# Kernel tuning notes

Hardware: AMD Instinct MI355X
Metric: run time of the kernel (lower is better)

The kernel has to match this reference:

```python
import jax, jax.numpy as jnp
from jax import lax
import numpy as np

C = 256
K = 3
PAD = 1


def _bilinear_sample(x, py, px):
    """Zero-padded bilinear sampling.
    x: [B,C,Hin,Win]; py,px: [B,Kt,H,W] float sample coords -> [B,C,Kt,H,W]."""
    B, Cc, Hin, Win = x.shape
    y0 = jnp.floor(py)
    x0 = jnp.floor(px)
    y1 = y0 + 1.0
    x1 = x0 + 1.0
    wy1 = py - y0
    wy0 = 1.0 - wy1
    wx1 = px - x0
    wx0 = 1.0 - wx1
    xf = x.reshape(B, Cc, Hin * Win)

    def corner(yi, xi, wy, wx):
        valid = (yi >= 0) & (yi < Hin) & (xi >= 0) & (xi < Win)
        yc = jnp.clip(yi, 0, Hin - 1).astype(jnp.int32)
        xc = jnp.clip(xi, 0, Win - 1).astype(jnp.int32)
        idx = yc * Win + xc  # [B,Kt,H,W]
        g = jax.vmap(lambda xb, ib: xb[:, ib])(xf, idx)  # [B,C,Kt,H,W]
        w = (wy * wx) * valid.astype(x.dtype)
        return g * w[:, None]

    return (corner(y0, x0, wy0, wx0) + corner(y0, x1, wy0, wx1)
            + corner(y1, x0, wy1, wx0) + corner(y1, x1, wy1, wx1))


def _arm_forward(x, w_off, b_off, w, b):
    B, Cc, H, W = x.shape
    # offset-predicting conv (standard 3x3, pad 1)
    off = lax.conv_general_dilated(
        x, w_off, window_strides=(1, 1), padding=[(PAD, PAD), (PAD, PAD)],
        dimension_numbers=('NCHW', 'OIHW', 'NCHW')) + b_off[None, :, None, None]
    off = off.reshape(B, K * K, 2, H, W)  # [:, k, 0]=dy, [:, k, 1]=dx (mmcv layout)
    ky, kx = jnp.meshgrid(jnp.arange(K), jnp.arange(K), indexing='ij')
    ky = ky.reshape(-1).astype(x.dtype)  # [9]
    kx = kx.reshape(-1).astype(x.dtype)
    base_y = jnp.arange(H, dtype=x.dtype)[None, None, :, None]
    base_x = jnp.arange(W, dtype=x.dtype)[None, None, None, :]
    py = base_y - PAD + ky[None, :, None, None] + off[:, :, 0]  # [B,9,H,W]
    px = base_x - PAD + kx[None, :, None, None] + off[:, :, 1]
    sampled = _bilinear_sample(x, py, px)  # [B,C,9,H,W]
    out = jnp.einsum('bckhw,ock->bohw', sampled, w.reshape(Cc, Cc, K * K))
    out = out + b[None, :, None, None]
    return jax.nn.sigmoid(out)


def setup_inputs() -> dict:
    key = jax.random.key(0)
    k1, k2, k3, k4 = jax.random.split(key, 4)
    B, H, W = 8, 64, 64
    x = jax.random.normal(k1, (B, C, H, W), dtype=jnp.float32)
    # offset conv params (mmcv zero-inits these; use small random to exercise sampling)
    w_off = jax.random.normal(k2, (2 * K * K, C, K, K), dtype=jnp.float32) * 0.01
    b_off = jnp.zeros((2 * K * K,), dtype=jnp.float32)
    # deformable conv weight/bias (kaiming-ish scale)
    scale = 1.0 / np.sqrt(C * K * K)
    w = jax.random.normal(k3, (C, C, K, K), dtype=jnp.float32) * scale
    b = jax.random.normal(k4, (C,), dtype=jnp.float32) * scale
    return {"Fstagei": x, "w_off": w_off, "b_off": b_off, "w": w, "b": b}


def reference(Fstagei, w_off, b_off, w, b):
    return _arm_forward(Fstagei, w_off, b_off, w, b)
```

## Files before the change

kernel.cpp:

```cpp
#include <hip/hip_runtime.h>

typedef unsigned short u16;
typedef unsigned int u32;
typedef __attribute__((ext_vector_type(8))) short short8;
typedef __attribute__((ext_vector_type(4))) float f32x4;

#define BB 8
#define CCH 256
#define HH 64
#define WW 64
#define HP 66
#define NPOS 4096
#define KTOT 2304

#define XT_BYTES   17842176ull
#define W2R_OFF    17842176ull
#define WOFF2_OFF  19021824ull
#define P_OFF      19169280ull
#define OFF2_OFF   40402944ull
#define WS_MIN     42762240ull

__device__ __forceinline__ float bf2f(u16 u) {
    union { u32 u; float f; } v; v.u = ((u32)u) << 16; return v.f;
}
__device__ __forceinline__ u16 f2bf(float f) {
    union { float f; u32 u; } v; v.f = f;
    u32 r = v.u + 0x7FFFu + ((v.u >> 16) & 1u);
    return (u16)(r >> 16);
}
__device__ __forceinline__ u32 pk2(float a, float b) {
    return (u32)f2bf(a) | ((u32)f2bf(b) << 16);
}
__device__ __forceinline__ u32 cvtpk(float lo, float hi) {
    u32 r;
    asm("v_cvt_pk_bf16_f32 %0, %1, %2" : "=v"(r) : "v"(lo), "v"(hi));
    return r;
}
__device__ __forceinline__ void bf2x2(u32 p, float& a, float& b) {
    union { u32 u; float f; } va, vb;
    va.u = p << 16; vb.u = p & 0xffff0000u;
    a = va.f; b = vb.f;
}
__device__ __forceinline__ void ldg_lds16(const u16* g, u16* l) {
    __builtin_amdgcn_global_load_lds((const __attribute__((address_space(1))) u32*)g,
                                     (__attribute__((address_space(3))) u32*)l, 16, 0, 0);
}

__global__ __launch_bounds__(256) void k_pre(const float* __restrict__ w, const float* __restrict__ w_off,
                                             const float* __restrict__ x,
                                             u16* __restrict__ W2r, u16* __restrict__ Woff2,
                                             u16* __restrict__ xT) {
    __shared__ __align__(16) float SH[4608];
    int bx = blockIdx.x;
    int t = threadIdx.x;
    if (bx < 256) {
        int o = bx;
        const float* src = w + (size_t)o * 2304;
#pragma unroll
        for (int j = 0; j < 9; ++j) SH[j * 256 + t] = src[j * 256 + t];
        __syncthreads();
        u16* dst = W2r + (size_t)o * 2304;
#pragma unroll
        for (int k = 0; k < 9; ++k) dst[k * 256 + t] = f2bf(SH[t * 9 + k]);
    } else if (bx == 256) {
        for (int o2 = 0; o2 < 32; ++o2) {
            if (o2 < 18) {
                const float* src = w_off + (size_t)o2 * 2304;
#pragma unroll
                for (int j = 0; j < 9; ++j) SH[j * 256 + t] = src[j * 256 + t];
                __syncthreads();
#pragma unroll
                for (int k = 0; k < 9; ++k) Woff2[(size_t)o2 * 2304 + k * 256 + t] = f2bf(SH[t * 9 + k]);
                __syncthreads();
            } else {
#pragma unroll
                for (int k = 0; k < 9; ++k) Woff2[(size_t)o2 * 2304 + k * 256 + t] = 0;
            }
        }
    } else if (bx < 777) {
        int idx = (bx - 257) * 4 + (t >> 6);
        int b = idx / 260, m = idx - b * 260;
        int y, xx;
        if (m < 66)       { y = 0;  xx = m; }
        else if (m < 132) { y = 65; xx = m - 66; }
        else if (m < 196) { y = m - 132 + 1; xx = 0; }
        else              { y = m - 196 + 1; xx = 65; }
        u16* p = xT + ((size_t)(b * HP + y) * HP + xx) * CCH + (t & 63) * 4;
        uint2 zz; zz.x = 0; zz.y = 0;
        *(uint2*)p = zz;
    } else {
        int idx = bx - 777;
        int b = idx & 7;
        int r = idx >> 3;
        int y = r & 63, c0 = (r >> 6) * 64;
        {
            int i = t >> 2, seg = t & 3;
            const float* src = x + (((size_t)(b * CCH + c0 + i) * HH + y) * WW) + seg * 16;
            float4 v0 = *(const float4*)(src);
            float4 v1 = *(const float4*)(src + 4);
            float4 v2 = *(const float4*)(src + 8);
            float4 v3 = *(const float4*)(src + 12);
            *(float4*)&SH[i * 72 + seg * 16]      = v0;
            *(float4*)&SH[i * 72 + seg * 16 + 4]  = v1;
            *(float4*)&SH[i * 72 + seg * 16 + 8]  = v2;
            *(float4*)&SH[i * 72 + seg * 16 + 12] = v3;
        }
        __syncthreads();
        {
            int xc = t >> 2, cs = t & 3;
            u16* dst = xT + (((size_t)(b * HP + y + 1) * HP) + (xc + 1)) * CCH + c0 + cs * 16;
            u32 p[8];
#pragma unroll
            for (int j = 0; j < 8; ++j)
                p[j] = pk2(SH[(cs * 16 + 2 * j) * 72 + xc], SH[(cs * 16 + 2 * j + 1) * 72 + xc]);
            uint4 d0, d1;
            d0.x = p[0]; d0.y = p[1]; d0.z = p[2]; d0.w = p[3];
            d1.x = p[4]; d1.y = p[5]; d1.z = p[6]; d1.w = p[7];
            *(uint4*)dst = d0;
            *(uint4*)(dst + 8) = d1;
        }
    }
}

__global__ __launch_bounds__(256) void k_offconv(const u16* __restrict__ xT,
                                                 const u16* __restrict__ Woff2,
                                                 float* __restrict__ P) {
    __shared__ __align__(16) u16 AS[2][2048];
    __shared__ __align__(16) u16 BS[2][8192];
    int b = blockIdx.x, k9 = blockIdx.y;
    int pos0 = blockIdx.z * 128;
    int ky = k9 / 3, kx = k9 % 3;
    int t = threadIdx.x, lane = t & 63, wv = t >> 6;

    int srow = lane >> 3;
    int sw8 = ((lane & 7) ^ srow) << 3;
    const u16* pA = Woff2 + (size_t)k9 * 256;
    const u16* pXb = xT + (size_t)b * HP * HP * CCH;

    f32x4 acc[2][2];
    f32x4 z = {0.f, 0.f, 0.f, 0.f};
    acc[0][0] = z; acc[0][1] = z; acc[1][0] = z; acc[1][1] = z;

    auto stage = [&](int cs, int d) {
        int koff = cs * 64;
        {
            int row = wv * 8 + srow;
            ldg_lds16(pA + (size_t)row * KTOT + koff + sw8, &AS[d][wv * 512]);
        }
#pragma unroll
        for (int i = 0; i < 4; ++i) {
            int inst = wv * 4 + i;
            int rowg = pos0 + inst * 8 + srow;
            int py_ = rowg >> 6, px_ = rowg & 63;
            const u16* g = pXb + (((size_t)(py_ + ky) * HP) + px_ + kx) * CCH + koff + sw8;
            ldg_lds16(g, &BS[d][inst * 512]);
        }
    };

    stage(0, 0);
    __syncthreads();

    int buf = 0;
    int m = lane & 15, q = lane >> 4, key = lane & 7;
    for (int cs = 0; cs < 4; ++cs) {
        if (cs < 3) stage(cs + 1, buf ^ 1);
#pragma unroll
        for (int j = 0; j < 2; ++j) {
            int slot8 = (((j * 4 + q) ^ key) << 3);
            short8 a0 = *(const short8*)&AS[buf][m * 64 + slot8];
            short8 a1 = *(const short8*)&AS[buf][(16 + m) * 64 + slot8];
            short8 b0 = *(const short8*)&BS[buf][(wv * 32 + m) * 64 + slot8];
            short8 b1 = *(const short8*)&BS[buf][(wv * 32 + 16 + m) * 64 + slot8];
            acc[0][0] = __builtin_amdgcn_mfma_f32_16x16x32_bf16(a0, b0, acc[0][0], 0, 0, 0);
            acc[0][1] = __builtin_amdgcn_mfma_f32_16x16x32_bf16(a0, b1, acc[0][1], 0, 0, 0);
            acc[1][0] = __builtin_amdgcn_mfma_f32_16x16x32_bf16(a1, b0, acc[1][0], 0, 0, 0);
            acc[1][1] = __builtin_amdgcn_mfma_f32_16x16x32_bf16(a1, b1, acc[1][1], 0, 0, 0);
        }
        __syncthreads();
        buf ^= 1;
    }
    int nn = lane & 15;
    float* Pp = P + (size_t)(b * 9 + k9) * 18 * NPOS;
#pragma unroll
    for (int ao = 0; ao < 2; ++ao)
#pragma unroll
        for (int bn = 0; bn < 2; ++bn) {
            int pos = pos0 + wv * 32 + bn * 16 + nn;
#pragma unroll
            for (int r = 0; r < 4; ++r) {
                int o = ao * 16 + q * 4 + r;
                if (o < 18) Pp[o * NPOS + pos] = acc[ao][bn][r];
            }
        }
}

__global__ __launch_bounds__(256) void k_reduce(const float* __restrict__ P,
                                                const float* __restrict__ b_off,
                                                float2* __restrict__ off2) {
    int b = blockIdx.x;
    int pos = blockIdx.y * 256 + threadIdx.x;
    float s[18];
#pragma unroll
    for (int o = 0; o < 18; ++o) s[o] = b_off[o];
    const float* Pp = P + (size_t)(b * 9) * 18 * NPOS + pos;
    for (int k9 = 0; k9 < 9; ++k9) {
#pragma unroll
        for (int o = 0; o < 18; ++o)
            s[o] += Pp[(k9 * 18 + o) * NPOS];
    }
#pragma unroll
    for (int op = 0; op < 9; ++op) {
        float2 v; v.x = s[2 * op]; v.y = s[2 * op + 1];
        off2[(((size_t)(b * 9 + op)) << 12) + pos] = v;
    }
}

__global__ __launch_bounds__(512, 2) void k_gemm(const u16* __restrict__ xT,
                                                 const float2* __restrict__ off2,
                                                 const u16* __restrict__ W2r,
                                                 const float* __restrict__ bias,
                                                 float* __restrict__ out) {
    __shared__ __align__(16) u16 AS[2][16384];
    __shared__ __align__(16) u16 BSF[128 * 264];
    int b = blockIdx.x;
    int pos0 = blockIdx.z * 128;
    int t = threadIdx.x, lane = t & 63, wv = t >> 6;
    int wr = wv >> 1, wc = wv & 1;

    int srow = lane >> 3;
    int sw8 = ((lane & 7) ^ srow) << 3;
    const u16* pA = W2r;

    int brow0 = t >> 3;
    int bcl = (t & 7) << 3;
    int bbase = b * HP * HP;

    f32x4 acc[4][4];
    f32x4 z = {0.f, 0.f, 0.f, 0.f};
#pragma unroll
    for (int i = 0; i < 4; ++i)
#pragma unroll
        for (int j = 0; j < 4; ++j) acc[i][j] = z;

    auto stageA = [&](int gs, int d) {
        int k9 = gs >> 2, cs = gs & 3;
        int koffA = k9 * 256 + cs * 64;
#pragma unroll
        for (int i = 0; i < 4; ++i) {
            int inst = wv * 4 + i;
            int row = inst * 8 + srow;
            ldg_lds16(pA + (size_t)row * KTOT + koffA + sw8, &AS[d][inst * 512]);
        }
    };

    const u16* gp[2][4];
    float wt[2][4];
    float2 fnext[2];
    uint4 gv[8];

    auto computeState = [&](int tap) {
#pragma unroll
        for (int ii = 0; ii < 2; ++ii) {
            int pos = pos0 + brow0 + (ii << 6);
            int y = pos >> 6, x = pos & 63;
            int ky = tap / 3, kx = tap - (tap / 3) * 3;
            float pyf = (float)(y - 1 + ky) + fnext[ii].x;
            float pxf = (float)(x - 1 + kx) + fnext[ii].y;
            float y0f = floorf(pyf), x0f = floorf(pxf);
            int y0 = (int)y0f, x0 = (int)x0f;
            int y1 = y0 + 1, x1 = x0 + 1;
            float wy1 = pyf - y0f, wy0 = 1.f - wy1;
            float wx1 = pxf - x0f, wx0 = 1.f - wx1;
            bool vy0 = (y0 >= 0) & (y0 < HH), vy1 = (y1 >= 0) & (y1 < HH);
            bool vx0 = (x0 >= 0) & (x0 < WW), vx1 = (x1 >= 0) & (x1 < WW);
            int yc0 = min(max(y0, 0), HH - 1), yc1 = min(max(y1, 0), HH - 1);
            int xc0 = min(max(x0, 0), WW - 1), xc1 = min(max(x1, 0), WW - 1);
            wt[ii][0] = (vy0 & vx0) ? wy0 * wx0 : 0.f;
            wt[ii][1] = (vy0 & vx1) ? wy0 * wx1 : 0.f;
            wt[ii][2] = (vy1 & vx0) ? wy1 * wx0 : 0.f;
            wt[ii][3] = (vy1 & vx1) ? wy1 * wx1 : 0.f;
            gp[ii][0] = xT + (size_t)(bbase + (yc0 + 1) * HP + xc0 + 1) * CCH + bcl;
            gp[ii][1] = xT + (size_t)(bbase + (yc0 + 1) * HP + xc1 + 1) * CCH + bcl;
            gp[ii][2] = xT + (size_t)(bbase + (yc1 + 1) * HP + xc0 + 1) * CCH + bcl;
            gp[ii][3] = xT + (size_t)(bbase + (yc1 + 1) * HP + xc1 + 1) * CCH + bcl;
        }
    };
    auto gatherRegion = [&](int rr) {
#pragma unroll
        for (int ii = 0; ii < 2; ++ii)
#pragma unroll
            for (int c = 0; c < 4; ++c)
                gv[ii * 4 + c] = *(const uint4*)(gp[ii][c] + rr * 64);
    };
    auto blendWrite = [&](int rr) {
#pragma unroll
        for (int ii = 0; ii < 2; ++ii) {
            int row = brow0 + (ii << 6);
            float v[8];
#pragma unroll
            for (int dw = 0; dw < 4; ++dw) {
                float a0, b0_, a1, b1_, a2, b2_, a3, b3_;
                bf2x2(((const u32*)&gv[ii * 4 + 0])[dw], a0, b0_);
                bf2x2(((const u32*)&gv[ii * 4 + 1])[dw], a1, b1_);
                bf2x2(((const u32*)&gv[ii * 4 + 2])[dw], a2, b2_);
                bf2x2(((const u32*)&gv[ii * 4 + 3])[dw], a3, b3_);
                v[2 * dw]     = wt[ii][0] * a0 + wt[ii][1] * a1 + wt[ii][2] * a2 + wt[ii][3] * a3;
                v[2 * dw + 1] = wt[ii][0] * b0_ + wt[ii][1] * b1_ + wt[ii][2] * b2_ + wt[ii][3] * b3_;
            }
            uint4 sv;
            sv.x = cvtpk(v[0], v[1]); sv.y = cvtpk(v[2], v[3]);
            sv.z = cvtpk(v[4], v[5]); sv.w = cvtpk(v[6], v[7]);
            *(uint4*)&BSF[row * 264 + rr * 64 + bcl] = sv;
        }
    };

    {
        fnext[0] = off2[((size_t)(b * 9 + 0) << 12) + pos0 + brow0];
        fnext[1] = off2[((size_t)(b * 9 + 0) << 12) + pos0 + brow0 + 64];
        computeState(0);
#pragma unroll
        for (int rr = 0; rr < 4; ++rr) {
            gatherRegion(rr);
            blendWrite(rr);
        }
        fnext[0] = off2[((size_t)(b * 9 + 1) << 12) + pos0 + brow0];
        fnext[1] = off2[((size_t)(b * 9 + 1) << 12) + pos0 + brow0 + 64];
        stageA(0, 0);
        asm volatile("s_waitcnt lgkmcnt(0)" ::: "memory");
    }

    int m = lane & 15, q = lane >> 4, key = lane & 7;
    for (int gs = 0; gs <= 35; ++gs) {
        int t9 = gs >> 2, cs = gs & 3, cur = gs & 1;
        if (gs >= 1 && gs <= 32) { asm volatile("s_waitcnt vmcnt(8)" ::: "memory"); }
        else                     { asm volatile("s_waitcnt vmcnt(0)" ::: "memory"); }
        __builtin_amdgcn_s_barrier();

        if (gs < 35) stageA(gs + 1, cur ^ 1);
        __builtin_amdgcn_sched_barrier(0);

        if (gs >= 1 && gs <= 32) {
            asm volatile("s_waitcnt vmcnt(4)" ::: "memory");
            blendWrite((cs + 3) & 3);
        }
        if (cs == 0 && t9 <= 7) computeState(t9 + 1);
        if (gs <= 31) {
            if (cs == 3 && t9 <= 6) {
                fnext[0] = off2[((size_t)(b * 9 + t9 + 2) << 12) + pos0 + brow0];
                fnext[1] = off2[((size_t)(b * 9 + t9 + 2) << 12) + pos0 + brow0 + 64];
            }
            gatherRegion(cs);
        }
        __builtin_amdgcn_sched_barrier(0);

#pragma unroll
        for (int j = 0; j < 2; ++j) {
            int slot8 = (((j * 4 + q) ^ key) << 3);
            int bchunk = (cs * 8 + j * 4 + q) << 3;
            short8 af[4], bfr[4];
#pragma unroll
            for (int ao = 0; ao < 4; ++ao)
                af[ao] = *(const short8*)&AS[cur][(wr * 64 + ao * 16 + m) * 64 + slot8];
#pragma unroll
            for (int bn = 0; bn < 4; ++bn)
                bfr[bn] = *(const short8*)&BSF[(wc * 64 + bn * 16 + m) * 264 + bchunk];
            __builtin_amdgcn_s_setprio(1);
#pragma unroll
            for (int ao = 0; ao < 4; ++ao)
#pragma unroll
                for (int bn = 0; bn < 4; ++bn)
                    acc[ao][bn] = __builtin_amdgcn_mfma_f32_16x16x32_bf16(af[ao], bfr[bn], acc[ao][bn], 0, 0, 0);
            __builtin_amdgcn_s_setprio(0);
        }
        asm volatile("s_waitcnt lgkmcnt(0)" ::: "memory");
    }

    int nn = lane & 15;
#pragma unroll
    for (int ao = 0; ao < 4; ++ao) {
        int ob = wr * 64 + ao * 16 + q * 4;
#pragma unroll
        for (int bn = 0; bn < 4; ++bn) {
            int pos = pos0 + wc * 64 + bn * 16 + nn;
#pragma unroll
            for (int r = 0; r < 4; ++r) {
                float v = acc[ao][bn][r] + bias[ob + r];
                float sg = 1.0f / (1.0f + __expf(-v));
                out[(size_t)((b * CCH + ob + r) * NPOS) + pos] = sg;
            }
        }
    }
}

extern "C" void kernel_launch(void* const* d_in, const int* in_sizes, int n_in,
                              void* d_out, int out_size, void* d_ws, size_t ws_size,
                              hipStream_t stream) {
    const float* x     = (const float*)d_in[0];
    const float* w_off = (const float*)d_in[1];
    const float* b_off = (const float*)d_in[2];
    const float* w     = (const float*)d_in[3];
    const float* bias  = (const float*)d_in[4];
    float* out = (float*)d_out;

    char* ws = (char*)d_ws;
    u16*    xT    = (u16*)ws;
    u16*    W2r   = (u16*)(ws + W2R_OFF);
    u16*    Woff2 = (u16*)(ws + WOFF2_OFF);
    float*  P     = (float*)(ws + P_OFF);
    float2* off2  = (float2*)(ws + OFF2_OFF);

    if (ws_size < WS_MIN) return;

    k_pre<<<2825, 256, 0, stream>>>(w, w_off, x, W2r, Woff2, xT);
    k_offconv<<<dim3(8, 9, 32), 256, 0, stream>>>(xT, Woff2, P);
    k_reduce<<<dim3(8, 16), 256, 0, stream>>>(P, b_off, off2);
    k_gemm<<<dim3(8, 1, 32), 512, 0, stream>>>(xT, off2, W2r, bias, out);
}
```

Baseline: 185.7 us.

## Halve GEMM position tile to 64 and use 32-wide K steps for more blocks

The deformable-conv GEMM kernel now processes 64 output positions per block instead of 128, and the K loop steps 32 channels at a time over 72 iterations instead of 64 over 36. The grid doubles to 512 blocks, shared memory per block is roughly halved, and the launch bound asks for 4 blocks per CU, with the aim of better occupancy and CU coverage on a grid that was only 256 blocks. In exchange each block reloads the full weight matrix for half as many positions, there are twice as many barriers and pipeline stages, and the old XOR swizzle on the A tile is removed, which may bring back LDS bank conflicts.

```diff
diff --git a/kernel.cpp b/kernel.cpp
--- a/kernel.cpp
+++ b/kernel.cpp
@@ -215,163 +215,139 @@
     }
 }
 
-__global__ __launch_bounds__(512, 2) void k_gemm(const u16* __restrict__ xT,
+__global__ __launch_bounds__(512, 4) void k_gemm(const u16* __restrict__ xT,
                                                  const float2* __restrict__ off2,
                                                  const u16* __restrict__ W2r,
                                                  const float* __restrict__ bias,
                                                  float* __restrict__ out) {
-    __shared__ __align__(16) u16 AS[2][16384];
-    __shared__ __align__(16) u16 BSF[128 * 264];
+    __shared__ __align__(16) u16 AS[2][8192];
+    __shared__ __align__(16) u16 BSF[64 * 264];
     int b = blockIdx.x;
-    int pos0 = blockIdx.z * 128;
+    int pos0 = blockIdx.z * 64;
     int t = threadIdx.x, lane = t & 63, wv = t >> 6;
     int wr = wv >> 1, wc = wv & 1;
 
-    int srow = lane >> 3;
-    int sw8 = ((lane & 7) ^ srow) << 3;
     const u16* pA = W2r;
-
-    int brow0 = t >> 3;
-    int bcl = (t & 7) << 3;
+    int brow = t >> 3;
+    int bcl = (t & 7) * 4;
     int bbase = b * HP * HP;
 
-    f32x4 acc[4][4];
+    f32x4 acc[4][2];
     f32x4 z = {0.f, 0.f, 0.f, 0.f};
 #pragma unroll
-    for (int i = 0; i < 4; ++i)
-#pragma unroll
-        for (int j = 0; j < 4; ++j) acc[i][j] = z;
+    for (int i = 0; i < 4; ++i) {
+        acc[i][0] = z; acc[i][1] = z;
+    }
 
     auto stageA = [&](int gs, int d) {
-        int k9 = gs >> 2, cs = gs & 3;
-        int koffA = k9 * 256 + cs * 64;
-#pragma unroll
-        for (int i = 0; i < 4; ++i) {
-            int inst = wv * 4 + i;
-            int row = inst * 8 + srow;
-            ldg_lds16(pA + (size_t)row * KTOT + koffA + sw8, &AS[d][inst * 512]);
-        }
-    };
-
-    const u16* gp[2][4];
-    float wt[2][4];
-    float2 fnext[2];
-    uint4 gv[8];
+        int koffA = gs * 32;
+#pragma unroll
+        for (int p = 0; p < 2; ++p) {
+            int row = p * 128 + wv * 16 + (lane >> 2);
+            ldg_lds16(pA + (size_t)row * KTOT + koffA + (lane & 3) * 8,
+                      &AS[d][p * 4096 + wv * 512]);
+        }
+    };
+
+    const u16* gp[4];
+    float wt[4];
+    float2 fnext;
+    uint2 gv[4];
 
     auto computeState = [&](int tap) {
-#pragma unroll
-        for (int ii = 0; ii < 2; ++ii) {
-            int pos = pos0 + brow0 + (ii << 6);
-            int y = pos >> 6, x = pos & 63;
-            int ky = tap / 3, kx = tap - (tap / 3) * 3;
-            float pyf = (float)(y - 1 + ky) + fnext[ii].x;
-            float pxf = (float)(x - 1 + kx) + fnext[ii].y;
-            float y0f = floorf(pyf), x0f = floorf(pxf);
-            int y0 = (int)y0f, x0 = (int)x0f;
-            int y1 = y0 + 1, x1 = x0 + 1;
-            float wy1 = pyf - y0f, wy0 = 1.f - wy1;
-            float wx1 = pxf - x0f, wx0 = 1.f - wx1;
-            bool vy0 = (y0 >= 0) & (y0 < HH), vy1 = (y1 >= 0) & (y1 < HH);
-            bool vx0 = (x0 >= 0) & (x0 < WW), vx1 = (x1 >= 0) & (x1 < WW);
-            int yc0 = min(max(y0, 0), HH - 1), yc1 = min(max(y1, 0), HH - 1);
-            int xc0 = min(max(x0, 0), WW - 1), xc1 = min(max(x1, 0), WW - 1);
-            wt[ii][0] = (vy0 & vx0) ? wy0 * wx0 : 0.f;
-            wt[ii][1] = (vy0 & vx1) ? wy0 * wx1 : 0.f;
-            wt[ii][2] = (vy1 & vx0) ? wy1 * wx0 : 0.f;
-            wt[ii][3] = (vy1 & vx1) ? wy1 * wx1 : 0.f;
-            gp[ii][0] = xT + (size_t)(bbase + (yc0 + 1) * HP + xc0 + 1) * CCH + bcl;
-            gp[ii][1] = xT + (size_t)(bbase + (yc0 + 1) * HP + xc1 + 1) * CCH + bcl;
-            gp[ii][2] = xT + (size_t)(bbase + (yc1 + 1) * HP + xc0 + 1) * CCH + bcl;
-            gp[ii][3] = xT + (size_t)(bbase + (yc1 + 1) * HP + xc1 + 1) * CCH + bcl;
-        }
+        int pos = pos0 + brow;
+        int y = pos >> 6, x = pos & 63;
+        int ky = tap / 3, kx = tap - (tap / 3) * 3;
+        float pyf = (float)(y - 1 + ky) + fnext.x;
+        float pxf = (float)(x - 1 + kx) + fnext.y;
+        float y0f = floorf(pyf), x0f = floorf(pxf);
+        int y0 = (int)y0f, x0 = (int)x0f;
+        int y1 = y0 + 1, x1 = x0 + 1;
+        float wy1 = pyf - y0f, wy0 = 1.f - wy1;
+        float wx1 = pxf - x0f, wx0 = 1.f - wx1;
+        bool vy0 = (y0 >= 0) & (y0 < HH), vy1 = (y1 >= 0) & (y1 < HH);
+        bool vx0 = (x0 >= 0) & (x0 < WW), vx1 = (x1 >= 0) & (x1 < WW);
+        int yc0 = min(max(y0, 0), HH - 1), yc1 = min(max(y1, 0), HH - 1);
+        int xc0 = min(max(x0, 0), WW - 1), xc1 = min(max(x1, 0), WW - 1);
+        wt[0] = (vy0 & vx0) ? wy0 * wx0 : 0.f;
+        wt[1] = (vy0 & vx1) ? wy0 * wx1 : 0.f;
+        wt[2] = (vy1 & vx0) ? wy1 * wx0 : 0.f;
+        wt[3] = (vy1 & vx1) ? wy1 * wx1 : 0.f;
+        gp[0] = xT + (size_t)(bbase + (yc0 + 1) * HP + xc0 + 1) * CCH + bcl;
+        gp[1] = xT + (size_t)(bbase + (yc0 + 1) * HP + xc1 + 1) * CCH + bcl;
+        gp[2] = xT + (size_t)(bbase + (yc1 + 1) * HP + xc0 + 1) * CCH + bcl;
+        gp[3] = xT + (size_t)(bbase + (yc1 + 1) * HP + xc1 + 1) * CCH + bcl;
     };
     auto gatherRegion = [&](int rr) {
 #pragma unroll
-        for (int ii = 0; ii < 2; ++ii)
-#pragma unroll
-            for (int c = 0; c < 4; ++c)
-                gv[ii * 4 + c] = *(const uint4*)(gp[ii][c] + rr * 64);
+        for (int c = 0; c < 4; ++c)
+            gv[c] = *(const uint2*)(gp[c] + rr * 32);
     };
     auto blendWrite = [&](int rr) {
-#pragma unroll
-        for (int ii = 0; ii < 2; ++ii) {
-            int row = brow0 + (ii << 6);
-            float v[8];
-#pragma unroll
-            for (int dw = 0; dw < 4; ++dw) {
-                float a0, b0_, a1, b1_, a2, b2_, a3, b3_;
-                bf2x2(((const u32*)&gv[ii * 4 + 0])[dw], a0, b0_);
-                bf2x2(((const u32*)&gv[ii * 4 + 1])[dw], a1, b1_);
-                bf2x2(((const u32*)&gv[ii * 4 + 2])[dw], a2, b2_);
-                bf2x2(((const u32*)&gv[ii * 4 + 3])[dw], a3, b3_);
-                v[2 * dw]     = wt[ii][0] * a0 + wt[ii][1] * a1 + wt[ii][2] * a2 + wt[ii][3] * a3;
-                v[2 * dw + 1] = wt[ii][0] * b0_ + wt[ii][1] * b1_ + wt[ii][2] * b2_ + wt[ii][3] * b3_;
-            }
-            uint4 sv;
-            sv.x = cvtpk(v[0], v[1]); sv.y = cvtpk(v[2], v[3]);
-            sv.z = cvtpk(v[4], v[5]); sv.w = cvtpk(v[6], v[7]);
-            *(uint4*)&BSF[row * 264 + rr * 64 + bcl] = sv;
-        }
+        float v[4];
+        float a0, b0_, a1, b1_, a2, b2_, a3, b3_;
+        bf2x2(gv[0].x, a0, b0_); bf2x2(gv[1].x, a1, b1_);
+        bf2x2(gv[2].x, a2, b2_); bf2x2(gv[3].x, a3, b3_);
+        v[0] = wt[0] * a0 + wt[1] * a1 + wt[2] * a2 + wt[3] * a3;
+        v[1] = wt[0] * b0_ + wt[1] * b1_ + wt[2] * b2_ + wt[3] * b3_;
+        bf2x2(gv[0].y, a0, b0_); bf2x2(gv[1].y, a1, b1_);
+        bf2x2(gv[2].y, a2, b2_); bf2x2(gv[3].y, a3, b3_);
+        v[2] = wt[0] * a0 + wt[1] * a1 + wt[2] * a2 + wt[3] * a3;
+        v[3] = wt[0] * b0_ + wt[1] * b1_ + wt[2] * b2_ + wt[3] * b3_;
+        uint2 sv;
+        sv.x = cvtpk(v[0], v[1]); sv.y = cvtpk(v[2], v[3]);
+        *(uint2*)&BSF[brow * 264 + rr * 32 + bcl] = sv;
     };
 
     {
-        fnext[0] = off2[((size_t)(b * 9 + 0) << 12) + pos0 + brow0];
-        fnext[1] = off2[((size_t)(b * 9 + 0) << 12) + pos0 + brow0 + 64];
+        fnext = off2[((size_t)(b * 9 + 0) << 12) + pos0 + brow];
         computeState(0);
 #pragma unroll
-        for (int rr = 0; rr < 4; ++rr) {
+        for (int rr = 0; rr < 8; ++rr) {
             gatherRegion(rr);
             blendWrite(rr);
         }
-        fnext[0] = off2[((size_t)(b * 9 + 1) << 12) + pos0 + brow0];
-        fnext[1] = off2[((size_t)(b * 9 + 1) << 12) + pos0 + brow0 + 64];
+        fnext = off2[((size_t)(b * 9 + 1) << 12) + pos0 + brow];
         stageA(0, 0);
         asm volatile("s_waitcnt lgkmcnt(0)" ::: "memory");
     }
 
-    int m = lane & 15, q = lane >> 4, key = lane & 7;
-    for (int gs = 0; gs <= 35; ++gs) {
-        int t9 = gs >> 2, cs = gs & 3, cur = gs & 1;
-        if (gs >= 1 && gs <= 32) { asm volatile("s_waitcnt vmcnt(8)" ::: "memory"); }
+    int m = lane & 15, q = lane >> 4;
+    for (int gs = 0; gs < 72; ++gs) {
+        int t9 = gs >> 3, cs = gs & 7, cur = gs & 1;
+        if (gs >= 1 && gs <= 64) { asm volatile("s_waitcnt vmcnt(4)" ::: "memory"); }
         else                     { asm volatile("s_waitcnt vmcnt(0)" ::: "memory"); }
         __builtin_amdgcn_s_barrier();
 
-        if (gs < 35) stageA(gs + 1, cur ^ 1);
+        if (gs < 71) stageA(gs + 1, cur ^ 1);
         __builtin_amdgcn_sched_barrier(0);
 
-        if (gs >= 1 && gs <= 32) {
-            asm volatile("s_waitcnt vmcnt(4)" ::: "memory");
-            blendWrite((cs + 3) & 3);
+        if (gs >= 1 && gs <= 64) {
+            asm volatile("s_waitcnt vmcnt(2)" ::: "memory");
+            blendWrite((cs + 7) & 7);
         }
         if (cs == 0 && t9 <= 7) computeState(t9 + 1);
-        if (gs <= 31) {
-            if (cs == 3 && t9 <= 6) {
-                fnext[0] = off2[((size_t)(b * 9 + t9 + 2) << 12) + pos0 + brow0];
-                fnext[1] = off2[((size_t)(b * 9 + t9 + 2) << 12) + pos0 + brow0 + 64];
-            }
+        if (gs <= 63) {
+            if (cs == 7 && t9 <= 6)
+                fnext = off2[((size_t)(b * 9 + t9 + 2) << 12) + pos0 + brow];
             gatherRegion(cs);
         }
         __builtin_amdgcn_sched_barrier(0);
 
-#pragma unroll
-        for (int j = 0; j < 2; ++j) {
-            int slot8 = (((j * 4 + q) ^ key) << 3);
-            int bchunk = (cs * 8 + j * 4 + q) << 3;
-            short8 af[4], bfr[4];
-#pragma unroll
-            for (int ao = 0; ao < 4; ++ao)
-                af[ao] = *(const short8*)&AS[cur][(wr * 64 + ao * 16 + m) * 64 + slot8];
-#pragma unroll
-            for (int bn = 0; bn < 4; ++bn)
-                bfr[bn] = *(const short8*)&BSF[(wc * 64 + bn * 16 + m) * 264 + bchunk];
-            __builtin_amdgcn_s_setprio(1);
-#pragma unroll
-            for (int ao = 0; ao < 4; ++ao)
-#pragma unroll
-                for (int bn = 0; bn < 4; ++bn)
-                    acc[ao][bn] = __builtin_amdgcn_mfma_f32_16x16x32_bf16(af[ao], bfr[bn], acc[ao][bn], 0, 0, 0);
-            __builtin_amdgcn_s_setprio(0);
-        }
+        short8 af[4], bfr[2];
+#pragma unroll
+        for (int ao = 0; ao < 4; ++ao)
+            af[ao] = *(const short8*)&AS[cur][(wr * 64 + ao * 16 + m) * 32 + q * 8];
+#pragma unroll
+        for (int bn = 0; bn < 2; ++bn)
+            bfr[bn] = *(const short8*)&BSF[(wc * 32 + bn * 16 + m) * 264 + cs * 32 + q * 8];
+        __builtin_amdgcn_s_setprio(1);
+#pragma unroll
+        for (int ao = 0; ao < 4; ++ao)
+#pragma unroll
+            for (int bn = 0; bn < 2; ++bn)
+                acc[ao][bn] = __builtin_amdgcn_mfma_f32_16x16x32_bf16(af[ao], bfr[bn], acc[ao][bn], 0, 0, 0);
+        __builtin_amdgcn_s_setprio(0);
         asm volatile("s_waitcnt lgkmcnt(0)" ::: "memory");
     }
 
@@ -380,8 +356,8 @@
     for (int ao = 0; ao < 4; ++ao) {
         int ob = wr * 64 + ao * 16 + q * 4;
 #pragma unroll
-        for (int bn = 0; bn < 4; ++bn) {
-            int pos = pos0 + wc * 64 + bn * 16 + nn;
+        for (int bn = 0; bn < 2; ++bn) {
+            int pos = pos0 + wc * 32 + bn * 16 + nn;
 #pragma unroll
             for (int r = 0; r < 4; ++r) {
                 float v = acc[ao][bn][r] + bias[ob + r];
@@ -414,5 +390,5 @@
     k_pre<<<2825, 256, 0, stream>>>(w, w_off, x, W2r, Woff2, xT);
     k_offconv<<<dim3(8, 9, 32), 256, 0, stream>>>(xT, Woff2, P);
     k_reduce<<<dim3(8, 16), 256, 0, stream>>>(P, b_off, off2);
-    k_gemm<<<dim3(8, 1, 32), 512, 0, stream>>>(xT, off2, W2r, bias, out);
-}
+    k_gemm<<<dim3(8, 1, 64), 512, 0, stream>>>(xT, off2, W2r, bias, out);
+}
```

Measured after the change: 202.1 us. 1.09x slower.

## Fuse offset conv split-K reduction into one kernel and reorder gemm MFMA before gather

Applied to the files above, without the earlier changes.

The offset convolution no longer splits the 9 kernel taps across blocks writing partials to a workspace buffer. Each block now loops over all 36 K-slices and writes the final offsets with bias directly, which removes the separate reduce kernel and the partial-sum traffic. The trade-off is fewer blocks (256 instead of 2304), so there is less parallelism and a longer serial loop per block. Separately, the main gemm now issues its MFMA block before the blend-write and gather phases in each iteration, to change how compute overlaps with memory.

```diff
diff --git a/kernel.cpp b/kernel.cpp
--- a/kernel.cpp
+++ b/kernel.cpp
@@ -16,13 +16,9 @@
 #define XT_BYTES   17842176ull
 #define W2R_OFF    17842176ull
 #define WOFF2_OFF  19021824ull
-#define P_OFF      19169280ull
 #define OFF2_OFF   40402944ull
 #define WS_MIN     42762240ull
 
-__device__ __forceinline__ float bf2f(u16 u) {
-    union { u32 u; float f; } v; v.u = ((u32)u) << 16; return v.f;
-}
 __device__ __forceinline__ u16 f2bf(float f) {
     union { float f; u32 u; } v; v.f = f;
     u32 r = v.u + 0x7FFFu + ((v.u >> 16) & 1u);
@@ -122,97 +118,82 @@
     }
 }
 
-__global__ __launch_bounds__(256) void k_offconv(const u16* __restrict__ xT,
-                                                 const u16* __restrict__ Woff2,
-                                                 float* __restrict__ P) {
+__global__ __launch_bounds__(256) void k_off2(const u16* __restrict__ xT,
+                                              const u16* __restrict__ Woff2,
+                                              const float* __restrict__ b_off,
+                                              float2* __restrict__ off2) {
     __shared__ __align__(16) u16 AS[2][2048];
     __shared__ __align__(16) u16 BS[2][8192];
-    int b = blockIdx.x, k9 = blockIdx.y;
-    int pos0 = blockIdx.z * 128;
-    int ky = k9 / 3, kx = k9 % 3;
+    int b = blockIdx.x;
+    int pos0 = blockIdx.y * 128;
     int t = threadIdx.x, lane = t & 63, wv = t >> 6;
 
     int srow = lane >> 3;
     int sw8 = ((lane & 7) ^ srow) << 3;
-    const u16* pA = Woff2 + (size_t)k9 * 256;
     const u16* pXb = xT + (size_t)b * HP * HP * CCH;
 
     f32x4 acc[2][2];
     f32x4 z = {0.f, 0.f, 0.f, 0.f};
     acc[0][0] = z; acc[0][1] = z; acc[1][0] = z; acc[1][1] = z;
 
-    auto stage = [&](int cs, int d) {
-        int koff = cs * 64;
+    auto stage = [&](int gs, int d) {
+        int t9 = gs >> 2, cs = gs & 3;
+        int ky = t9 / 3, kx = t9 - (t9 / 3) * 3;
+        int koff = t9 * 256 + cs * 64;
         {
             int row = wv * 8 + srow;
-            ldg_lds16(pA + (size_t)row * KTOT + koff + sw8, &AS[d][wv * 512]);
+            ldg_lds16(Woff2 + (size_t)row * KTOT + koff + sw8, &AS[d][wv * 512]);
         }
 #pragma unroll
         for (int i = 0; i < 4; ++i) {
             int inst = wv * 4 + i;
             int rowg = pos0 + inst * 8 + srow;
             int py_ = rowg >> 6, px_ = rowg & 63;
-            const u16* g = pXb + (((size_t)(py_ + ky) * HP) + px_ + kx) * CCH + koff + sw8;
+            const u16* g = pXb + (((size_t)(py_ + ky) * HP) + px_ + kx) * CCH + cs * 64 + sw8;
             ldg_lds16(g, &BS[d][inst * 512]);
         }
     };
 
     stage(0, 0);
-    __syncthreads();
-
-    int buf = 0;
+
     int m = lane & 15, q = lane >> 4, key = lane & 7;
-    for (int cs = 0; cs < 4; ++cs) {
-        if (cs < 3) stage(cs + 1, buf ^ 1);
+    for (int gs = 0; gs < 36; ++gs) {
+        int cur = gs & 1;
+        asm volatile("s_waitcnt vmcnt(0)" ::: "memory");
+        __builtin_amdgcn_s_barrier();
+        if (gs < 35) stage(gs + 1, cur ^ 1);
 #pragma unroll
         for (int j = 0; j < 2; ++j) {
             int slot8 = (((j * 4 + q) ^ key) << 3);
-            short8 a0 = *(const short8*)&AS[buf][m * 64 + slot8];
-            short8 a1 = *(const short8*)&AS[buf][(16 + m) * 64 + slot8];
-            short8 b0 = *(const short8*)&BS[buf][(wv * 32 + m) * 64 + slot8];
-            short8 b1 = *(const short8*)&BS[buf][(wv * 32 + 16 + m) * 64 + slot8];
+            short8 a0 = *(const short8*)&AS[cur][m * 64 + slot8];
+            short8 a1 = *(const short8*)&AS[cur][(16 + m) * 64 + slot8];
+            short8 b0 = *(const short8*)&BS[cur][(wv * 32 + m) * 64 + slot8];
+            short8 b1 = *(const short8*)&BS[cur][(wv * 32 + 16 + m) * 64 + slot8];
             acc[0][0] = __builtin_amdgcn_mfma_f32_16x16x32_bf16(a0, b0, acc[0][0], 0, 0, 0);
             acc[0][1] = __builtin_amdgcn_mfma_f32_16x16x32_bf16(a0, b1, acc[0][1], 0, 0, 0);
             acc[1][0] = __builtin_amdgcn_mfma_f32_16x16x32_bf16(a1, b0, acc[1][0], 0, 0, 0);
             acc[1][1] = __builtin_amdgcn_mfma_f32_16x16x32_bf16(a1, b1, acc[1][1], 0, 0, 0);
         }
-        __syncthreads();
-        buf ^= 1;
-    }
+        asm volatile("s_waitcnt lgkmcnt(0)" ::: "memory");
+    }
+
     int nn = lane & 15;
-    float* Pp = P + (size_t)(b * 9 + k9) * 18 * NPOS;
 #pragma unroll
     for (int ao = 0; ao < 2; ++ao)
 #pragma unroll
         for (int bn = 0; bn < 2; ++bn) {
             int pos = pos0 + wv * 32 + bn * 16 + nn;
 #pragma unroll
-            for (int r = 0; r < 4; ++r) {
-                int o = ao * 16 + q * 4 + r;
-                if (o < 18) Pp[o * NPOS + pos] = acc[ao][bn][r];
-            }
-        }
-}
-
-__global__ __launch_bounds__(256) void k_reduce(const float* __restrict__ P,
-                                                const float* __restrict__ b_off,
-                                                float2* __restrict__ off2) {
-    int b = blockIdx.x;
-    int pos = blockIdx.y * 256 + threadIdx.x;
-    float s[18];
-#pragma unroll
-    for (int o = 0; o < 18; ++o) s[o] = b_off[o];
-    const float* Pp = P + (size_t)(b * 9) * 18 * NPOS + pos;
-    for (int k9 = 0; k9 < 9; ++k9) {
-#pragma unroll
-        for (int o = 0; o < 18; ++o)
-            s[o] += Pp[(k9 * 18 + o) * NPOS];
-    }
-#pragma unroll
-    for (int op = 0; op < 9; ++op) {
-        float2 v; v.x = s[2 * op]; v.y = s[2 * op + 1];
-        off2[(((size_t)(b * 9 + op)) << 12) + pos] = v;
-    }
+            for (int rp = 0; rp < 2; ++rp) {
+                int o = ao * 16 + q * 4 + rp * 2;
+                if (o < 18) {
+                    float2 v;
+                    v.x = acc[ao][bn][rp * 2]     + b_off[o];
+                    v.y = acc[ao][bn][rp * 2 + 1] + b_off[o + 1];
+                    off2[(((size_t)(b * 9 + (o >> 1))) << 12) + pos] = v;
+                }
+            }
+        }
 }
 
 __global__ __launch_bounds__(512, 2) void k_gemm(const u16* __restrict__ xT,
@@ -339,6 +320,27 @@
         if (gs < 35) stageA(gs + 1, cur ^ 1);
         __builtin_amdgcn_sched_barrier(0);
 
+#pragma unroll
+        for (int j = 0; j < 2; ++j) {
+            int slot8 = (((j * 4 + q) ^ key) << 3);
+            int bchunk = (cs * 8 + j * 4 + q) << 3;
+            short8 af[4], bfr[4];
+#pragma unroll
+            for (int ao = 0; ao < 4; ++ao)
+                af[ao] = *(const short8*)&AS[cur][(wr * 64 + ao * 16 + m) * 64 + slot8];
+#pragma unroll
+            for (int bn = 0; bn < 4; ++bn)
+                bfr[bn] = *(const short8*)&BSF[(wc * 64 + bn * 16 + m) * 264 + bchunk];
+            __builtin_amdgcn_s_setprio(1);
+#pragma unroll
+            for (int ao = 0; ao < 4; ++ao)
+#pragma unroll
+                for (int bn = 0; bn < 4; ++bn)
+                    acc[ao][bn] = __builtin_amdgcn_mfma_f32_16x16x32_bf16(af[ao], bfr[bn], acc[ao][bn], 0, 0, 0);
+            __builtin_amdgcn_s_setprio(0);
+        }
+        __builtin_amdgcn_sched_barrier(0);
+
         if (gs >= 1 && gs <= 32) {
             asm volatile("s_waitcnt vmcnt(4)" ::: "memory");
             blendWrite((cs + 3) & 3);
@@ -350,27 +352,6 @@
                 fnext[1] = off2[((size_t)(b * 9 + t9 + 2) << 12) + pos0 + brow0 + 64];
             }
             gatherRegion(cs);
-        }
-        __builtin_amdgcn_sched_barrier(0);
-
-#pragma unroll
-        for (int j = 0; j < 2; ++j) {
-            int slot8 = (((j * 4 + q) ^ key) << 3);
-            int bchunk = (cs * 8 + j * 4 + q) << 3;
-            short8 af[4], bfr[4];
-#pragma unroll
-            for (int ao = 0; ao < 4; ++ao)
-                af[ao] = *(const short8*)&AS[cur][(wr * 64 + ao * 16 + m) * 64 + slot8];
-#pragma unroll
-            for (int bn = 0; bn < 4; ++bn)
-                bfr[bn] = *(const short8*)&BSF[(wc * 64 + bn * 16 + m) * 264 + bchunk];
-            __builtin_amdgcn_s_setprio(1);
-#pragma unroll
-            for (int ao = 0; ao < 4; ++ao)
-#pragma unroll
-                for (int bn = 0; bn < 4; ++bn)
-                    acc[ao][bn] = __builtin_amdgcn_mfma_f32_16x16x32_bf16(af[ao], bfr[bn], acc[ao][bn], 0, 0, 0);
-            __builtin_amdgcn_s_setprio(0);
         }
         asm volatile("s_waitcnt lgkmcnt(0)" ::: "memory");
     }
@@ -406,13 +387,11 @@
     u16*    xT    = (u16*)ws;
     u16*    W2r   = (u16*)(ws + W2R_OFF);
     u16*    Woff2 = (u16*)(ws + WOFF2_OFF);
-    float*  P     = (float*)(ws + P_OFF);
     float2* off2  = (float2*)(ws + OFF2_OFF);
 
     if (ws_size < WS_MIN) return;
 
     k_pre<<<2825, 256, 0, stream>>>(w, w_off, x, W2r, Woff2, xT);
-    k_offconv<<<dim3(8, 9, 32), 256, 0, stream>>>(xT, Woff2, P);
-    k_reduce<<<dim3(8, 16), 256, 0, stream>>>(P, b_off, off2);
+    k_off2<<<dim3(8, 32), 256, 0, stream>>>(xT, Woff2, b_off, off2);
     k_gemm<<<dim3(8, 1, 32), 512, 0, stream>>>(xT, off2, W2r, bias, out);
 }
```

After: 197.4 us. +6.3%, slower.
